# Kernel optimization log

Measured on AMD Instinct MI355X. Metric: run time of the kernel, lower is better.

The kernel has to match this reference:

```python
import jax, jax.numpy as jnp
import numpy as np

B, T, C = 2, 2048, 1024
H, D = 16, 64


def setup_inputs() -> dict:
    key = jax.random.key(0)
    k1, k2, k3 = jax.random.split(key, 3)
    x = jax.random.normal(k1, (B, T, C), dtype=jnp.float32)
    w_qkv = jax.random.normal(k2, (C, 3 * H * D), dtype=jnp.float32) * (C ** -0.5)
    w_proj = jax.random.normal(k3, (H * D, C), dtype=jnp.float32) * ((H * D) ** -0.5)
    sink_logit = jnp.zeros((H,), dtype=jnp.float32)
    return {"x": x, "w_qkv": w_qkv, "w_proj": w_proj, "sink_logit": sink_logit}


def reference(x, w_qkv, w_proj, sink_logit):
    b, t, c = x.shape
    qkv = x @ w_qkv                                  # [B,T,3HD]
    q, k, v = jnp.split(qkv, 3, axis=-1)
    # [B,H,T,D]
    q = q.reshape(b, t, H, D).transpose(0, 2, 1, 3)
    k = k.reshape(b, t, H, D).transpose(0, 2, 1, 3)
    v = v.reshape(b, t, H, D).transpose(0, 2, 1, 3)

    scale = 1.0 / jnp.sqrt(jnp.asarray(D, dtype=x.dtype))
    scores = jnp.einsum('bhqd,bhkd->bhqk', q, k) * scale   # [B,H,T,T]
    neg_inf = jnp.finfo(x.dtype).min
    causal = jnp.tril(jnp.ones((t, t), dtype=bool))
    scores = jnp.where(causal[None, None], scores, neg_inf)

    # sink column: per-head learnable logit b (added post-scale, V is zero)
    sink = jnp.broadcast_to(sink_logit.reshape(1, H, 1, 1), (b, H, t, 1)).astype(x.dtype)
    aug = jnp.concatenate([sink, scores], axis=-1)          # [B,H,T,T+1]
    attn = jax.nn.softmax(aug, axis=-1)
    # sink V is zero, so drop the sink column for the value contraction
    y = jnp.einsum('bhqk,bhkd->bhqd', attn[..., 1:], v)     # [B,H,T,D]
    y = y.transpose(0, 2, 1, 3).reshape(b, t, H * D)
    return y @ w_proj
```

## Files before the change

kernel.cpp:

```cpp
#include <hip/hip_runtime.h>
#include <hip/hip_bf16.h>
#include <stdint.h>

#define B_ 2
#define T_ 2048
#define C_ 1024
#define H_ 16
#define D_ 64

typedef __attribute__((ext_vector_type(8))) short short8;
typedef __attribute__((ext_vector_type(4))) float floatx4;

__device__ __forceinline__ float bf2f(uint16_t b) {
    return __uint_as_float(((uint32_t)b) << 16);
}
__device__ __forceinline__ uint16_t f2b(float f) {
    __hip_bfloat16 h = __float2bfloat16(f);
    return *(uint16_t*)&h;
}
__device__ __forceinline__ void glds16(const uint16_t* g, uint16_t* l) {
    __builtin_amdgcn_global_load_lds(
        (const __attribute__((address_space(1))) uint32_t*)g,
        (__attribute__((address_space(3))) uint32_t*)l, 16, 0, 0);
}

__global__ void canon_x(const float* __restrict__ in, uint16_t* __restrict__ out,
                        int n) {
    int i = (blockIdx.x * 256 + threadIdx.x) * 4;
    if (i >= n) return;
    float4 v = *(const float4*)(in + i);
    out[i + 0] = f2b(v.x);
    out[i + 1] = f2b(v.y);
    out[i + 2] = f2b(v.z);
    out[i + 3] = f2b(v.w);
}

__global__ void transpose_conv(const float* __restrict__ in, uint16_t* __restrict__ out,
                               int R, int W) {
    __shared__ uint16_t tile[32][33];
    int tx = threadIdx.x, ty = threadIdx.y;
    int c0 = blockIdx.x * 32, r0 = blockIdx.y * 32;
    #pragma unroll
    for (int i = 0; i < 32; i += 8)
        tile[ty + i][tx] = f2b(in[(size_t)(r0 + ty + i) * W + (c0 + tx)]);
    __syncthreads();
    #pragma unroll
    for (int i = 0; i < 32; i += 8)
        out[(size_t)(c0 + ty + i) * R + (r0 + tx)] = tile[tx][ty + i];
}

template <bool OUT_F32>
__global__ __launch_bounds__(256, 2)
void gemm_bt(const uint16_t* __restrict__ A, const uint16_t* __restrict__ Bt,
             void* __restrict__ Cv, int M, int N, int K) {
    __shared__ uint16_t As[2][128][64];
    __shared__ uint16_t Bs[2][128][64];
    int tid = threadIdx.x;
    int w = tid >> 6, lane = tid & 63;
    int quad = lane >> 4, l16 = lane & 15;
    int wr = (w >> 1) * 64, wc = (w & 1) * 64;

    int nwg = gridDim.x;
    int wg = (blockIdx.x & 7) * (nwg >> 3) + (blockIdx.x >> 3);
    int nby = N >> 7;
    int row0 = (wg / nby) * 128;
    int col0 = (wg % nby) * 128;

    int sr = w * 32 + (lane >> 3);
    int gsc = ((lane & 7) ^ (lane >> 3)) * 8;
    uint16_t* lA = &As[0][sr][(lane & 7) * 8];
    uint16_t* lB = &Bs[0][sr][(lane & 7) * 8];
    const size_t LBUF = 128 * 64;
    const uint16_t* gA = A + (size_t)(row0 + sr) * K + gsc;
    const uint16_t* gB = Bt + (size_t)(col0 + sr) * K + gsc;

    floatx4 acc[4][4];
    #pragma unroll
    for (int i = 0; i < 4; i++)
        #pragma unroll
        for (int j = 0; j < 4; j++)
            acc[i][j] = (floatx4){0.f, 0.f, 0.f, 0.f};

#define STAGE_(buf, k0)                                                     \
    {                                                                       \
        _Pragma("unroll") for (int j = 0; j < 4; j++) {                     \
            glds16(gA + (size_t)j * 8 * K + (k0), lA + (buf)*LBUF + j * 8 * 64); \
            glds16(gB + (size_t)j * 8 * K + (k0), lB + (buf)*LBUF + j * 8 * 64); \
        }                                                                   \
    }

    int NT = K >> 6;
    STAGE_(0, 0);
    __syncthreads();

    for (int t = 0; t < NT; ++t) {
        int cur = t & 1;
        if (t + 1 < NT) STAGE_(cur ^ 1, (t + 1) << 6);
        #pragma unroll
        for (int kk = 0; kk < 2; kk++) {
            int s = ((kk * 4 + quad) ^ (l16 & 7)) * 8;
            short8 af[4], bf[4];
            #pragma unroll
            for (int i = 0; i < 4; i++)
                af[i] = *(const short8*)&As[cur][wr + i * 16 + l16][s];
            #pragma unroll
            for (int j = 0; j < 4; j++)
                bf[j] = *(const short8*)&Bs[cur][wc + j * 16 + l16][s];
            #pragma unroll
            for (int i = 0; i < 4; i++)
                #pragma unroll
                for (int j = 0; j < 4; j++)
                    acc[i][j] = __builtin_amdgcn_mfma_f32_16x16x32_bf16(
                        af[i], bf[j], acc[i][j], 0, 0, 0);
        }
        __syncthreads();
    }
#undef STAGE_

    #pragma unroll
    for (int i = 0; i < 4; i++) {
        #pragma unroll
        for (int j = 0; j < 4; j++) {
            int rbase = row0 + wr + i * 16 + quad * 4;
            int cg = col0 + wc + j * 16 + l16;
            #pragma unroll
            for (int r = 0; r < 4; r++) {
                if (OUT_F32)
                    ((float*)Cv)[(size_t)(rbase + r) * N + cg] = acc[i][j][r];
                else
                    ((uint16_t*)Cv)[(size_t)(rbase + r) * N + cg] = f2b(acc[i][j][r]);
            }
        }
    }
}

__global__ __launch_bounds__(256, 2)
void attn_mfma(const uint16_t* __restrict__ qkv,
               const float* __restrict__ sink,
               uint16_t* __restrict__ y) {
    __shared__ uint16_t Ks[2][64][72];
    __shared__ uint16_t Vt[2][64][72];
    __shared__ uint16_t Pl[4][32][72];

    int tid = threadIdx.x;
    int w = tid >> 6, lane = tid & 63;
    int quad = lane >> 4, l16 = lane & 15;

    int id = blockIdx.x;
    int pair = id >> 5, bh = id & 31;
    int b = bh >> 4, h = bh & 15;
    int strip = (w < 2) ? (31 - pair) : pair;
    int q0w = strip * 64 + (w & 1) * 32;
    int ktiles = 32 - pair;
    int myktiles = strip + 1;

    const uint16_t* qkv_b = qkv + (size_t)b * T_ * 3072;

    short8 qf[2][2];
    #pragma unroll
    for (int qt = 0; qt < 2; qt++) {
        int qrow = q0w + qt * 16 + l16;
        #pragma unroll
        for (int kd = 0; kd < 2; kd++) {
            uint4 raw = *(const uint4*)(qkv_b + (size_t)qrow * 3072 + h * 64 +
                                        kd * 32 + quad * 8);
            const uint16_t* rp = (const uint16_t*)&raw;
            short8 f;
            #pragma unroll
            for (int j = 0; j < 8; j++)
                f[j] = (short)f2b(bf2f(rp[j]) * 0.125f);
            qf[qt][kd] = f;
        }
    }

    float m_s[2], l_s[2];
    m_s[0] = m_s[1] = sink[h];
    l_s[0] = l_s[1] = 1.0f;
    floatx4 acc_o[2][4];
    #pragma unroll
    for (int qt = 0; qt < 2; qt++)
        #pragma unroll
        for (int dt = 0; dt < 4; dt++)
            acc_o[qt][dt] = (floatx4){0.f, 0.f, 0.f, 0.f};

    int t2 = tid >> 3;
    int dg = tid & 7;
    const uint16_t* kgp = qkv_b + 1024 + h * 64 + (size_t)(2 * t2) * 3072 + dg * 8;
    const uint16_t* vgp = kgp + 1024;
    int vcw = 2 * (t2 ^ (4 * dg));

    uint4 kr0 = *(const uint4*)(kgp);
    uint4 kr1 = *(const uint4*)(kgp + 3072);
    uint4 vr0 = *(const uint4*)(vgp);
    uint4 vr1 = *(const uint4*)(vgp + 3072);
    {
        *(uint4*)&Ks[0][2 * t2][dg * 8] = kr0;
        *(uint4*)&Ks[0][2 * t2 + 1][dg * 8] = kr1;
        const uint16_t* a0 = (const uint16_t*)&vr0;
        const uint16_t* a1 = (const uint16_t*)&vr1;
        #pragma unroll
        for (int j = 0; j < 8; j++)
            *(uint32_t*)&Vt[0][dg * 8 + j][vcw] =
                (uint32_t)a0[j] | ((uint32_t)a1[j] << 16);
    }
    if (ktiles > 1) {
        kr0 = *(const uint4*)(kgp + 64 * 3072);
        kr1 = *(const uint4*)(kgp + 64 * 3072 + 3072);
        vr0 = *(const uint4*)(vgp + 64 * 3072);
        vr1 = *(const uint4*)(vgp + 64 * 3072 + 3072);
    }
    __syncthreads();

    for (int kt = 0; kt < ktiles; kt++) {
        int cur = kt & 1;
        if (kt + 1 < ktiles) {
            *(uint4*)&Ks[cur ^ 1][2 * t2][dg * 8] = kr0;
            *(uint4*)&Ks[cur ^ 1][2 * t2 + 1][dg * 8] = kr1;
            const uint16_t* a0 = (const uint16_t*)&vr0;
            const uint16_t* a1 = (const uint16_t*)&vr1;
            #pragma unroll
            for (int j = 0; j < 8; j++)
                *(uint32_t*)&Vt[cur ^ 1][dg * 8 + j][vcw] =
                    (uint32_t)a0[j] | ((uint32_t)a1[j] << 16);
        }
        if (kt + 2 < ktiles) {
            size_t off = (size_t)(kt + 2) * 64 * 3072;
            kr0 = *(const uint4*)(kgp + off);
            kr1 = *(const uint4*)(kgp + off + 3072);
            vr0 = *(const uint4*)(vgp + off);
            vr1 = *(const uint4*)(vgp + off + 3072);
        }
        if (kt < myktiles) {
            short8 kf[4][2];
            #pragma unroll
            for (int rt = 0; rt < 4; rt++) {
                kf[rt][0] = *(const short8*)&Ks[cur][rt * 16 + l16][quad * 8];
                kf[rt][1] = *(const short8*)&Ks[cur][rt * 16 + l16][32 + quad * 8];
            }
            short8 vf[2][4];
            #pragma unroll
            for (int kb = 0; kb < 2; kb++)
                #pragma unroll
                for (int dt = 0; dt < 4; dt++) {
                    int d = dt * 16 + l16;
                    int col = 2 * (((kb * 16) + quad * 4) ^ (4 * (d >> 3)));
                    vf[kb][dt] = *(const short8*)&Vt[cur][d][col];
                }
            #pragma unroll
            for (int qt = 0; qt < 2; qt++) {
                floatx4 acc_s[4];
                #pragma unroll
                for (int rt = 0; rt < 4; rt++)
                    acc_s[rt] = (floatx4){0.f, 0.f, 0.f, 0.f};
                #pragma unroll
                for (int rt = 0; rt < 4; rt++) {
                    acc_s[rt] = __builtin_amdgcn_mfma_f32_16x16x32_bf16(
                        kf[rt][0], qf[qt][0], acc_s[rt], 0, 0, 0);
                    acc_s[rt] = __builtin_amdgcn_mfma_f32_16x16x32_bf16(
                        kf[rt][1], qf[qt][1], acc_s[rt], 0, 0, 0);
                }
                if (kt == strip) {
                    int qg = q0w + qt * 16 + l16;
                    #pragma unroll
                    for (int rt = 0; rt < 4; rt++) {
                        int kg = kt * 64 + rt * 16 + quad * 4;
                        #pragma unroll
                        for (int r = 0; r < 4; r++)
                            if (kg + r > qg) acc_s[rt][r] = -1e30f;
                    }
                }
                float mx = -1e30f;
                #pragma unroll
                for (int rt = 0; rt < 4; rt++)
                    #pragma unroll
                    for (int r = 0; r < 4; r++) mx = fmaxf(mx, acc_s[rt][r]);
                mx = fmaxf(mx, __shfl_xor(mx, 16));
                mx = fmaxf(mx, __shfl_xor(mx, 32));
                float mnew = fmaxf(m_s[qt], mx);
                float alpha = __expf(m_s[qt] - mnew);
                m_s[qt] = mnew;
                float psum = 0.f;
                #pragma unroll
                for (int rt = 0; rt < 4; rt++) {
                    float p0 = __expf(acc_s[rt][0] - mnew);
                    float p1 = __expf(acc_s[rt][1] - mnew);
                    float p2 = __expf(acc_s[rt][2] - mnew);
                    float p3 = __expf(acc_s[rt][3] - mnew);
                    psum += (p0 + p1) + (p2 + p3);
                    uint2 pk;
                    pk.x = (uint32_t)f2b(p0) | ((uint32_t)f2b(p1) << 16);
                    pk.y = (uint32_t)f2b(p2) | ((uint32_t)f2b(p3) << 16);
                    *(uint2*)&Pl[w][qt * 16 + l16][rt * 16 + quad * 4] = pk;
                }
                psum += __shfl_xor(psum, 16);
                psum += __shfl_xor(psum, 32);
                l_s[qt] = l_s[qt] * alpha + psum;
                #pragma unroll
                for (int r = 0; r < 4; r++) {
                    float ar = __shfl(alpha, (lane & 48) | (quad * 4 + r));
                    #pragma unroll
                    for (int dt = 0; dt < 4; dt++) acc_o[qt][dt][r] *= ar;
                }
                #pragma unroll
                for (int kb = 0; kb < 2; kb++) {
                    short8 pf = *(const short8*)&Pl[w][qt * 16 + l16][kb * 32 + quad * 8];
                    #pragma unroll
                    for (int dt = 0; dt < 4; dt++)
                        acc_o[qt][dt] = __builtin_amdgcn_mfma_f32_16x16x32_bf16(
                            pf, vf[kb][dt], acc_o[qt][dt], 0, 0, 0);
                }
            }
        }
        __syncthreads();
    }

    #pragma unroll
    for (int qt = 0; qt < 2; qt++) {
        #pragma unroll
        for (int r = 0; r < 4; r++) {
            float lr = __shfl(l_s[qt], (lane & 48) | (quad * 4 + r));
            float inv = 1.0f / lr;
            int qg = q0w + qt * 16 + quad * 4 + r;
            uint16_t* yp = y + (size_t)(b * T_ + qg) * 1024 + h * 64;
            #pragma unroll
            for (int dt = 0; dt < 4; dt++)
                yp[dt * 16 + l16] = f2b(acc_o[qt][dt][r] * inv);
        }
    }
}

extern "C" void kernel_launch(void* const* d_in, const int* in_sizes, int n_in,
                              void* d_out, int out_size, void* d_ws, size_t ws_size,
                              hipStream_t stream) {
    const float* x      = (const float*)d_in[0];
    const float* w_qkv  = (const float*)d_in[1];
    const float* w_proj = (const float*)d_in[2];
    const float* sink   = (const float*)d_in[3];
    float* out          = (float*)d_out;

    char* ws = (char*)d_ws;
    uint16_t* wt_qkv  = (uint16_t*)ws;
    uint16_t* wt_proj = (uint16_t*)(ws + 6291456);
    uint16_t* x_c     = (uint16_t*)(ws + 8388608);
    uint16_t* qkv     = (uint16_t*)(ws + 16777216);
    uint16_t* yb      = (uint16_t*)(ws + 41943040);

    canon_x<<<4194304 / 1024, 256, 0, stream>>>(x, x_c, 4194304);
    transpose_conv<<<dim3(3072 / 32, 1024 / 32), dim3(32, 8), 0, stream>>>(
        w_qkv, wt_qkv, 1024, 3072);
    transpose_conv<<<dim3(1024 / 32, 1024 / 32), dim3(32, 8), 0, stream>>>(
        w_proj, wt_proj, 1024, 1024);

    gemm_bt<false><<<dim3(768), 256, 0, stream>>>(
        x_c, wt_qkv, qkv, 4096, 3072, 1024);

    attn_mfma<<<dim3(16 * 32), 256, 0, stream>>>(qkv, sink, yb);

    gemm_bt<true><<<dim3(256), 256, 0, stream>>>(
        yb, wt_proj, out, 4096, 1024, 1024);
}
```

Before: 197.8 us.

## Triple-buffer GEMM LDS with BK=32 and explicit vmcnt-based pipelining

The projection GEMM drops from a double-buffered BK=64 LDS pipeline to a triple-buffered BK=32 pipeline with prefetch depth two. Each step now waits on vmcnt and issues a raw s_barrier instead of __syncthreads. The smaller LDS footprint allows launch bounds of 3 blocks per CU, raising occupancy. In exchange there are twice as many loop iterations and barriers, and the XOR swizzle is narrowed to a 4-chunk pattern.

```diff
diff --git a/kernel.cpp b/kernel.cpp
--- a/kernel.cpp
+++ b/kernel.cpp
@@ -50,11 +50,11 @@
 }
 
 template <bool OUT_F32>
-__global__ __launch_bounds__(256, 2)
+__global__ __launch_bounds__(256, 3)
 void gemm_bt(const uint16_t* __restrict__ A, const uint16_t* __restrict__ Bt,
              void* __restrict__ Cv, int M, int N, int K) {
-    __shared__ uint16_t As[2][128][64];
-    __shared__ uint16_t Bs[2][128][64];
+    __shared__ uint16_t As[3][128][32];
+    __shared__ uint16_t Bs[3][128][32];
     int tid = threadIdx.x;
     int w = tid >> 6, lane = tid & 63;
     int quad = lane >> 4, l16 = lane & 15;
@@ -66,11 +66,10 @@
     int row0 = (wg / nby) * 128;
     int col0 = (wg % nby) * 128;
 
-    int sr = w * 32 + (lane >> 3);
-    int gsc = ((lane & 7) ^ (lane >> 3)) * 8;
-    uint16_t* lA = &As[0][sr][(lane & 7) * 8];
-    uint16_t* lB = &Bs[0][sr][(lane & 7) * 8];
-    const size_t LBUF = 128 * 64;
+    int sr = w * 32 + (lane >> 2);
+    int gsc = ((lane & 3) ^ ((lane >> 2) & 3)) * 8;
+    uint16_t* lA0 = &As[0][sr][(lane & 3) * 8];
+    uint16_t* lB0 = &Bs[0][sr][(lane & 3) * 8];
     const uint16_t* gA = A + (size_t)(row0 + sr) * K + gsc;
     const uint16_t* gB = Bt + (size_t)(col0 + sr) * K + gsc;
 
@@ -81,41 +80,56 @@
         for (int j = 0; j < 4; j++)
             acc[i][j] = (floatx4){0.f, 0.f, 0.f, 0.f};
 
-#define STAGE_(buf, k0)                                                     \
+#define STAGE3_(bs_, t_)                                                    \
     {                                                                       \
-        _Pragma("unroll") for (int j = 0; j < 4; j++) {                     \
-            glds16(gA + (size_t)j * 8 * K + (k0), lA + (buf)*LBUF + j * 8 * 64); \
-            glds16(gB + (size_t)j * 8 * K + (k0), lB + (buf)*LBUF + j * 8 * 64); \
-        }                                                                   \
-    }
-
-    int NT = K >> 6;
-    STAGE_(0, 0);
-    __syncthreads();
-
+        const uint16_t* ga_ = gA + (size_t)(t_) * 32;                       \
+        const uint16_t* gb_ = gB + (size_t)(t_) * 32;                       \
+        uint16_t* la_ = lA0 + (bs_) * 4096;                                 \
+        uint16_t* lb_ = lB0 + (bs_) * 4096;                                 \
+        glds16(ga_, la_);                                                   \
+        glds16(ga_ + 16 * K, la_ + 512);                                    \
+        glds16(gb_, lb_);                                                   \
+        glds16(gb_ + 16 * K, lb_ + 512);                                    \
+    }
+
+    int NT = K >> 5;
+    STAGE3_(0, 0);
+    STAGE3_(1, 1);
+    asm volatile("s_waitcnt vmcnt(4)" ::: "memory");
+    __builtin_amdgcn_s_barrier();
+
+    const uint16_t* Ab = &As[0][0][0];
+    const uint16_t* Bb = &Bs[0][0][0];
+    int s = (quad ^ (l16 & 3)) * 8;
+    int bc = 0, bs = 2;
     for (int t = 0; t < NT; ++t) {
-        int cur = t & 1;
-        if (t + 1 < NT) STAGE_(cur ^ 1, (t + 1) << 6);
-        #pragma unroll
-        for (int kk = 0; kk < 2; kk++) {
-            int s = ((kk * 4 + quad) ^ (l16 & 7)) * 8;
-            short8 af[4], bf[4];
-            #pragma unroll
-            for (int i = 0; i < 4; i++)
-                af[i] = *(const short8*)&As[cur][wr + i * 16 + l16][s];
+        if (t + 2 < NT) STAGE3_(bs, t + 2);
+        __builtin_amdgcn_sched_barrier(0);
+        const uint16_t* Ac = Ab + bc * 4096;
+        const uint16_t* Bc = Bb + bc * 4096;
+        short8 af[4], bfr[4];
+        #pragma unroll
+        for (int i = 0; i < 4; i++)
+            af[i] = *(const short8*)&Ac[(wr + i * 16 + l16) * 32 + s];
+        #pragma unroll
+        for (int j = 0; j < 4; j++)
+            bfr[j] = *(const short8*)&Bc[(wc + j * 16 + l16) * 32 + s];
+        #pragma unroll
+        for (int i = 0; i < 4; i++)
             #pragma unroll
             for (int j = 0; j < 4; j++)
-                bf[j] = *(const short8*)&Bs[cur][wc + j * 16 + l16][s];
-            #pragma unroll
-            for (int i = 0; i < 4; i++)
-                #pragma unroll
-                for (int j = 0; j < 4; j++)
-                    acc[i][j] = __builtin_amdgcn_mfma_f32_16x16x32_bf16(
-                        af[i], bf[j], acc[i][j], 0, 0, 0);
-        }
-        __syncthreads();
-    }
-#undef STAGE_
+                acc[i][j] = __builtin_amdgcn_mfma_f32_16x16x32_bf16(
+                    af[i], bfr[j], acc[i][j], 0, 0, 0);
+        if (t + 2 < NT) {
+            asm volatile("s_waitcnt vmcnt(4)" ::: "memory");
+        } else {
+            asm volatile("s_waitcnt vmcnt(0)" ::: "memory");
+        }
+        __builtin_amdgcn_s_barrier();
+        bc = (bc == 2) ? 0 : bc + 1;
+        bs = (bs == 2) ? 0 : bs + 1;
+    }
+#undef STAGE3_
 
     #pragma unroll
     for (int i = 0; i < 4; i++) {
```

New measurement: 196.3 us. No clear change (-0.8%).
